# Optimization experiments

Measured on AMD Instinct MI355X. Metric: run time of the kernel, lower is better.

Reference implementation:

```python
import jax, jax.numpy as jnp
import numpy as np

P, D, K, E, ITERS, THRESH, NCLS = 16, 384, 16, 8, 10, 0.9, 1000


def _forward(x, pw, pb, ln_g, ln_b, pos, qw, qb, kw, kb, vw, vb,
             ew, eb, nw, nb, m1w, m1b, m2w, m2b, fbw, fbb, fgw, fgb, cw, cb):
    B, C, H, W = x.shape
    Hp, Wp = H // P, W // P
    # patch embedding: conv(k=s=P) == reshape + matmul; (c, ph, pw) ordering matches conv weight layout
    xp = x.reshape(B, C, Hp, P, Wp, P).transpose(0, 2, 4, 1, 3, 5).reshape(B, Hp * Wp, C * P * P)
    patches = xp @ pw + pb                                    # [B, N, D]
    # layer norm (eps=1e-5)
    mu = patches.mean(-1, keepdims=True)
    var = patches.var(-1, keepdims=True)
    pn = (patches - mu) / jnp.sqrt(var + 1e-5) * ln_g + ln_b
    # k-means (Lloyd, fixed iters, deterministic evenly-spaced init)
    N = pn.shape[1]
    init_idx = jnp.linspace(0, N - 1, K).astype(jnp.int32)
    centers0 = pn[:, init_idx]                                # [B, K, D]
    pn_sq = jnp.sum(pn * pn, -1)                              # [B, N]

    def kstep(centers, _):
        d2 = (pn_sq[:, :, None]
              - 2.0 * jnp.einsum('bnd,bkd->bnk', pn, centers)
              + jnp.sum(centers * centers, -1)[:, None, :])   # [B, N, K]
        oh = jax.nn.one_hot(jnp.argmin(d2, -1), K, dtype=pn.dtype)
        counts = oh.sum(1)                                    # [B, K]
        new = jnp.einsum('bnk,bnd->bkd', oh, pn) / jnp.maximum(counts, 1.0)[:, :, None]
        new = jnp.where(counts[:, :, None] > 0, new, centers)
        return new, None

    clusters, _ = jax.lax.scan(kstep, centers0, None, length=ITERS)  # [B, K, D]
    # attention over clusters
    clusters = clusters + pos
    Q = clusters @ qw + qb
    Kt = clusters @ kw + kb
    V = clusters @ vw + vb
    attn = jax.nn.softmax(jnp.einsum('bqd,bkd->bqk', Q, Kt) / jnp.sqrt(jnp.float32(D)), -1)
    clusters = jnp.einsum('bqk,bkd->bqd', attn, V)
    # hypergraph laplacian
    hw = jax.nn.softmax(clusters @ ew + eb, axis=1)           # [B, K, E], softmax over nodes
    Dd = hw.sum(1)                                            # [B, E]
    Hm = hw.transpose(0, 2, 1)                                # [B, E, K]
    M = (Dd ** -0.5)[:, :, None] * Hm                         # D^{-1/2} H
    L = jnp.eye(E, dtype=clusters.dtype) - jnp.einsum('bek,bfk->bef', M, Hm)  # [B, E, E]
    L = jnp.pad(L, ((0, 0), (0, K - E), (0, K - E)))          # pad to [B, K, K]
    clusters = jnp.einsum('bij,bjd->bid', L, clusters)
    clusters = clusters @ nw + nb
    # non-linear propagation MLP (exact GELU, torch default)
    clusters = jax.nn.gelu(clusters @ m1w + m1b, approximate=False) @ m2w + m2b
    # adaptive node collapse: mask from ORIGINAL clusters, sequential in-place merges
    nrm = jnp.maximum(jnp.linalg.norm(clusters, axis=-1, keepdims=True), 1e-12)
    nc = clusters / nrm
    sim = jnp.einsum('bqd,bkd->bqk', nc, nc)
    mask_any = jnp.any(sim > THRESH, axis=0)                  # [K, K]: merge pair if ANY batch exceeds
    for i in range(K):                                        # small fixed K; matches sequential torch loop
        for j in range(i + 1, K):
            cond = mask_any[i, j]
            merged = (clusters[:, i] + clusters[:, j]) * 0.5
            clusters = clusters.at[:, i].set(jnp.where(cond, merged, clusters[:, i]))
            clusters = clusters.at[:, j].set(jnp.where(cond, merged, clusters[:, j]))
    # feedback modulation
    g = clusters.mean(1)                                      # [B, D]
    fb = g @ fbw + fbb
    gate = jax.nn.sigmoid(g @ fgw + fgb)                      # [B, 1]
    clusters = clusters + fb[:, None, :] * gate[:, None, :]
    return clusters.reshape(B, -1) @ cw + cb                  # [B, num_classes]


def setup_inputs() -> dict:
    key = jax.random.key(0)
    ks = jax.random.split(key, 16)
    Wm = lambda k, *s: jax.random.normal(k, s, jnp.float32) * 0.02
    z = lambda *s: jnp.zeros(s, jnp.float32)
    return {
        'x': jax.random.normal(ks[0], (128, 3, 224, 224), jnp.float32),
        'pw': Wm(ks[1], 3 * P * P, D), 'pb': z(D),
        'ln_g': jnp.ones((D,), jnp.float32), 'ln_b': z(D),
        'pos': Wm(ks[2], K, D),
        'qw': Wm(ks[3], D, D), 'qb': z(D),
        'kw': Wm(ks[4], D, D), 'kb': z(D),
        'vw': Wm(ks[5], D, D), 'vb': z(D),
        'ew': Wm(ks[6], D, E), 'eb': z(E),
        'nw': Wm(ks[7], D, D), 'nb': z(D),
        'm1w': Wm(ks[8], D, D), 'm1b': z(D),
        'm2w': Wm(ks[9], D, D), 'm2b': z(D),
        'fbw': Wm(ks[10], D, D), 'fbb': z(D),
        'fgw': Wm(ks[11], D, 1), 'fgb': z(1),
        'cw': Wm(ks[12], D * K, NCLS), 'cb': z(NCLS),
    }


def reference(x, pw, pb, ln_g, ln_b, pos, qw, qb, kw, kb, vw, vb,
              ew, eb, nw, nb, m1w, m1b, m2w, m2b, fbw, fbb, fgw, fgb, cw, cb):
    return _forward(x, pw, pb, ln_g, ln_b, pos, qw, qb, kw, kb, vw, vb,
                    ew, eb, nw, nb, m1w, m1b, m2w, m2b, fbw, fbb, fgw, fgb, cw, cb)
```

## Files before the change

kernel.cpp:

```cpp
#include <hip/hip_runtime.h>
#include <math.h>

#define NBATCH 128
#define NPTS   196
#define DIN    768
#define DM     384
#define KCL    16
#define NEXP   8
#define NITER  10
#define NCLS   1000

__global__ __launch_bounds__(256) void init_kernel(const float* __restrict__ cb,
                                                   float* __restrict__ out,
                                                   int* __restrict__ mask) {
    int idx = blockIdx.x * 256 + threadIdx.x;
    if (idx < NBATCH * NCLS) {
        out[idx] = cb[idx % NCLS];
    } else if (idx < NBATCH * NCLS + 256) {
        mask[idx - NBATCH * NCLS] = 0;
    }
}

__global__ __launch_bounds__(256) void patch_ln_kernel(
        const float* __restrict__ x, const float* __restrict__ pw,
        const float* __restrict__ pb, const float* __restrict__ lng,
        const float* __restrict__ lnb, float* __restrict__ pn,
        float* __restrict__ pnsq) {
    __shared__ float As[32 * 32];
    __shared__ float Ws[32 * DM];
    const int tid  = threadIdx.x;
    const int m0   = blockIdx.x * 32;
    const int arow = tid >> 3, akg = tid & 7;
    const int m    = m0 + arow;
    const int bi   = m / NPTS, n = m - bi * NPTS;
    const int nh   = n / 14, nwp = n - nh * 14;
    const float* xb = x + (size_t)bi * 150528 + (size_t)(nh * 16) * 224 + nwp * 16;
    const int rg = tid >> 5, cg = tid & 31;

    float acc[4][12];
#pragma unroll
    for (int r = 0; r < 4; ++r)
#pragma unroll
        for (int j = 0; j < 12; ++j) acc[r][j] = 0.f;

    const float4* pw4 = (const float4*)pw;
    for (int kci = 0; kci < 24; ++kci) {
        {
            int k = kci * 32 + akg * 4;
            int c = k >> 8, py = (k >> 4) & 15, px = k & 15;
            float4 xv = *(const float4*)(xb + c * 50176 + py * 224 + px);
            As[(akg * 4 + 0) * 32 + arow] = xv.x;
            As[(akg * 4 + 1) * 32 + arow] = xv.y;
            As[(akg * 4 + 2) * 32 + arow] = xv.z;
            As[(akg * 4 + 3) * 32 + arow] = xv.w;
        }
#pragma unroll
        for (int t = 0; t < 12; ++t) {
            int s = tid + t * 256;
            ((float4*)Ws)[s] = pw4[kci * 3072 + s];
        }
        __syncthreads();
#pragma unroll 8
        for (int kk = 0; kk < 32; ++kk) {
            float4 a = *(const float4*)&As[kk * 32 + rg * 4];
            float w[12];
            *(float4*)&w[0] = *(const float4*)&Ws[kk * DM + cg * 12];
            *(float4*)&w[4] = *(const float4*)&Ws[kk * DM + cg * 12 + 4];
            *(float4*)&w[8] = *(const float4*)&Ws[kk * DM + cg * 12 + 8];
            float ar[4] = {a.x, a.y, a.z, a.w};
#pragma unroll
            for (int r = 0; r < 4; ++r)
#pragma unroll
                for (int j = 0; j < 12; ++j) acc[r][j] += ar[r] * w[j];
        }
        __syncthreads();
    }

    float gvv[12], bvv[12], pbv[12];
#pragma unroll
    for (int j4 = 0; j4 < 3; ++j4) {
        *(float4*)&pbv[j4 * 4] = *(const float4*)(pb + cg * 12 + j4 * 4);
        *(float4*)&gvv[j4 * 4] = *(const float4*)(lng + cg * 12 + j4 * 4);
        *(float4*)&bvv[j4 * 4] = *(const float4*)(lnb + cg * 12 + j4 * 4);
    }
#pragma unroll
    for (int r = 0; r < 4; ++r) {
        float vloc[12];
        float s = 0.f;
#pragma unroll
        for (int j = 0; j < 12; ++j) { vloc[j] = acc[r][j] + pbv[j]; s += vloc[j]; }
#pragma unroll
        for (int off = 16; off >= 1; off >>= 1) s += __shfl_xor(s, off);
        float mu = s * (1.0f / DM);
        float q = 0.f;
#pragma unroll
        for (int j = 0; j < 12; ++j) { float dd = vloc[j] - mu; q += dd * dd; }
#pragma unroll
        for (int off = 16; off >= 1; off >>= 1) q += __shfl_xor(q, off);
        float rstd = rsqrtf(q * (1.0f / DM) + 1e-5f);
        float ov[12];
        float ssq = 0.f;
#pragma unroll
        for (int j = 0; j < 12; ++j) {
            float p = (vloc[j] - mu) * rstd * gvv[j] + bvv[j];
            ov[j] = p; ssq += p * p;
        }
#pragma unroll
        for (int off = 16; off >= 1; off >>= 1) ssq += __shfl_xor(ssq, off);
        int mr = m0 + rg * 4 + r;
        float* dst = pn + (size_t)mr * DM + cg * 12;
        *(float4*)(dst)     = *(float4*)&ov[0];
        *(float4*)(dst + 4) = *(float4*)&ov[4];
        *(float4*)(dst + 8) = *(float4*)&ov[8];
        if (cg == 0) pnsq[mr] = ssq;
    }
}

__global__ __launch_bounds__(256) void kmeans_init_kernel(
        const float* __restrict__ pn, float* __restrict__ cent,
        float* __restrict__ csq, int* __restrict__ cnt) {
    const int b = blockIdx.x, tid = threadIdx.x;
    const float* pnb = pn + (size_t)b * NPTS * DM;
    float* cb = cent + (size_t)b * KCL * DM;
    for (int i = tid; i < KCL * DM / 4; i += 256) {
        int k = i / (DM / 4), d4 = i - k * (DM / 4);
        ((float4*)cb)[i] = ((const float4*)(pnb + (size_t)(13 * k) * DM))[d4];
    }
    if (tid < 128) {
        int k = tid >> 3, sub = tid & 7;
        const float* row = pnb + (size_t)(13 * k) * DM + sub * 48;
        float ss = 0.f;
        for (int d = 0; d < 48; d += 4) {
            float4 v = *(const float4*)(row + d);
            ss += v.x * v.x + v.y * v.y + v.z * v.z + v.w * v.w;
        }
#pragma unroll
        for (int off = 4; off >= 1; off >>= 1) ss += __shfl_xor(ss, off);
        if (sub == 0) csq[b * KCL + k] = ss;
    }
    if (tid < KCL) cnt[b * KCL + tid] = 0;
}

__global__ __launch_bounds__(256) void kmeans_assign_kernel(
        const float* __restrict__ pn, const float* __restrict__ pnsq,
        const float* __restrict__ cent, const float* __restrict__ csq,
        int* __restrict__ asn, int* __restrict__ cnt) {
    __shared__ float cs[KCL * DM];
    __shared__ float cq[KCL];
    const int b = blockIdx.y, tile = blockIdx.x, tid = threadIdx.x;
    const float* cb = cent + (size_t)b * KCL * DM;
    for (int i = tid; i < KCL * DM / 4; i += 256)
        ((float4*)cs)[i] = ((const float4*)cb)[i];
    if (tid < KCL) cq[tid] = csq[b * KCL + tid];
    __syncthreads();

    const int p = tid >> 3, sub = tid & 7;
    const int n = tile * 32 + p;
    if (n >= NPTS) return;
    const float4* prow = (const float4*)(pn + ((size_t)b * NPTS + n) * DM);

    float acc[KCL];
#pragma unroll
    for (int k = 0; k < KCL; ++k) acc[k] = 0.f;
#pragma unroll 2
    for (int i = 0; i < 12; ++i) {
        const int d4 = sub + 8 * i;
        float4 pv = prow[d4];
#pragma unroll
        for (int k = 0; k < KCL; ++k) {
            const float4 c = *(const float4*)&cs[k * DM + d4 * 4];
            acc[k] += pv.x * c.x + pv.y * c.y + pv.z * c.z + pv.w * c.w;
        }
    }
#pragma unroll
    for (int k = 0; k < KCL; ++k) {
        float a = acc[k];
        a += __shfl_xor(a, 1);
        a += __shfl_xor(a, 2);
        a += __shfl_xor(a, 4);
        acc[k] = a;
    }
    if (sub == 0) {
        const float mp = pnsq[b * NPTS + n];
        float best = (mp - 2.0f * acc[0]) + cq[0];
        int bk = 0;
#pragma unroll
        for (int k = 1; k < KCL; ++k) {
            float v = (mp - 2.0f * acc[k]) + cq[k];
            if (v < best) { best = v; bk = k; }
        }
        asn[b * NPTS + n] = bk;
        atomicAdd(&cnt[b * KCL + bk], 1);
    }
}

__global__ __launch_bounds__(256) void kmeans_update_kernel(
        const float* __restrict__ pn, const int* __restrict__ asn,
        int* __restrict__ cnt, float* __restrict__ cent,
        float* __restrict__ csq) {
    __shared__ unsigned long long msk[4];
    __shared__ float red[4];
    const int b = blockIdx.y, k = blockIdx.x, tid = threadIdx.x;

    int a = -1;
    if (tid < NPTS) a = asn[b * NPTS + tid];
    unsigned long long bal = __ballot(a == k);
    if ((tid & 63) == 0) msk[tid >> 6] = bal;
    __syncthreads();

    const int c = cnt[b * KCL + k];
    float sx = 0.f, sy = 0.f;
    const float* pnb = pn + (size_t)b * NPTS * DM + 2 * tid;
    if (tid < 192) {
#pragma unroll
        for (int w = 0; w < 4; ++w) {
            unsigned long long m = msk[w];
            while (m) {
                int nn = w * 64 + (int)__builtin_ctzll(m);
                m &= m - 1;
                float2 v = *(const float2*)(pnb + (size_t)nn * DM);
                sx += v.x; sy += v.y;
            }
        }
    }
    float* cr = cent + ((size_t)b * KCL + k) * DM + 2 * tid;
    float nx = 0.f, ny = 0.f;
    if (tid < 192) {
        if (c > 0) {
            float inv = 1.0f / (float)c;
            nx = sx * inv; ny = sy * inv;
        } else {
            nx = cr[0]; ny = cr[1];
        }
        cr[0] = nx; cr[1] = ny;
    }
    float ss = nx * nx + ny * ny;
#pragma unroll
    for (int off = 32; off >= 1; off >>= 1) ss += __shfl_xor(ss, off);
    if ((tid & 63) == 0) red[tid >> 6] = ss;
    __syncthreads();
    if (tid == 0) {
        csq[b * KCL + k] = red[0] + red[1] + red[2] + red[3];
        cnt[b * KCL + k] = 0;
    }
}

__global__ __launch_bounds__(256) void kmeans_finalize_kernel(
        float* __restrict__ cent, const float* __restrict__ pos) {
    int i = blockIdx.x * 256 + threadIdx.x;
    int within = i % (KCL * DM / 4);
    float4 cv = ((const float4*)cent)[i];
    float4 pv = ((const float4*)pos)[within];
    cv.x += pv.x; cv.y += pv.y; cv.z += pv.z; cv.w += pv.w;
    ((float4*)cent)[i] = cv;
}

template <int ACT>
__global__ __launch_bounds__(256) void gemm_kernel(
        const float* __restrict__ A, const float* __restrict__ W,
        const float* __restrict__ bias, float* __restrict__ out,
        int M, int N, int Kd) {
    __shared__ float As[32 * 32];
    __shared__ float Ws[32 * 128];
    const int n0 = blockIdx.x * 128;
    const int m0 = blockIdx.y * 32;
    const int tid = threadIdx.x;
    const int rg = tid >> 5, cg = tid & 31;
    const int arow = tid >> 3, akg = tid & 7;
    float acc[4][4];
#pragma unroll
    for (int r = 0; r < 4; ++r)
#pragma unroll
        for (int j = 0; j < 4; ++j) acc[r][j] = 0.f;

    for (int kc = 0; kc < Kd; kc += 32) {
        float4 av = *(const float4*)(A + (size_t)(m0 + arow) * Kd + kc + akg * 4);
        As[(akg * 4 + 0) * 32 + arow] = av.x;
        As[(akg * 4 + 1) * 32 + arow] = av.y;
        As[(akg * 4 + 2) * 32 + arow] = av.z;
        As[(akg * 4 + 3) * 32 + arow] = av.w;
#pragma unroll
        for (int t = 0; t < 4; ++t) {
            int s = tid + t * 256;
            int kk = s >> 5, c4i = s & 31;
            *(float4*)&Ws[kk * 128 + c4i * 4] =
                *(const float4*)(W + (size_t)(kc + kk) * N + n0 + c4i * 4);
        }
        __syncthreads();
#pragma unroll 16
        for (int kk = 0; kk < 32; ++kk) {
            float4 a = *(const float4*)&As[kk * 32 + rg * 4];
            float4 w = *(const float4*)&Ws[kk * 128 + cg * 4];
            float ar[4] = {a.x, a.y, a.z, a.w};
            float wr[4] = {w.x, w.y, w.z, w.w};
#pragma unroll
            for (int r = 0; r < 4; ++r)
#pragma unroll
                for (int j = 0; j < 4; ++j) acc[r][j] += ar[r] * wr[j];
        }
        __syncthreads();
    }
    float4 bv = *(const float4*)(bias + n0 + cg * 4);
    float bvr[4] = {bv.x, bv.y, bv.z, bv.w};
#pragma unroll
    for (int r = 0; r < 4; ++r) {
        float o[4];
#pragma unroll
        for (int j = 0; j < 4; ++j) {
            float v = acc[r][j] + bvr[j];
            if (ACT == 1) v = 0.5f * v * (1.0f + erff(v * 0.70710678118654752440f));
            o[j] = v;
        }
        *(float4*)(out + (size_t)(m0 + rg * 4 + r) * N + n0 + cg * 4) = *(float4*)&o[0];
    }
}

__global__ __launch_bounds__(256) void attn_spectral_kernel(
        const float* __restrict__ Qg, const float* __restrict__ Kg,
        const float* __restrict__ Vg, const float* __restrict__ ew,
        const float* __restrict__ eb, float* __restrict__ c2) {
    __shared__ float Qs[KCL * 388];
    __shared__ float Ks[KCL * 388];
    __shared__ float Ss[KCL * 17];
    __shared__ float hws[KCL * 9];
    __shared__ float rds[NEXP];
    __shared__ float Ls[NEXP * NEXP];
    const int b = blockIdx.x, tid = threadIdx.x;
    for (int idx = tid; idx < KCL * DM; idx += 256) {
        int i = idx / DM, d = idx - i * DM;
        size_t g = (size_t)b * KCL * DM + idx;
        Qs[i * 388 + d] = Qg[g];
        Ks[i * 388 + d] = Kg[g];
    }
    __syncthreads();
    {
        int i = tid >> 4, j = tid & 15;
        float acc = 0.f;
        for (int d = 0; d < DM; d += 4) {
            float4 q = *(const float4*)&Qs[i * 388 + d];
            float4 k = *(const float4*)&Ks[j * 388 + d];
            acc += q.x * k.x + q.y * k.y + q.z * k.z + q.w * k.w;
        }
        float s = acc / sqrtf((float)DM);
        float mx = s;
#pragma unroll
        for (int off = 8; off >= 1; off >>= 1) mx = fmaxf(mx, __shfl_xor(mx, off));
        float p = expf(s - mx);
        float sm = p;
#pragma unroll
        for (int off = 8; off >= 1; off >>= 1) sm += __shfl_xor(sm, off);
        Ss[i * 17 + j] = p / sm;
    }
    __syncthreads();
    for (int idx = tid; idx < KCL * DM; idx += 256) {
        int i = idx / DM, d = idx - i * DM;
        Ks[i * 388 + d] = Vg[(size_t)b * KCL * DM + idx];
    }
    __syncthreads();
    for (int idx = tid; idx < KCL * DM; idx += 256) {
        int i = idx / DM, d = idx - i * DM;
        float acc = 0.f;
#pragma unroll
        for (int j = 0; j < KCL; ++j) acc += Ss[i * 17 + j] * Ks[j * 388 + d];
        Qs[i * 388 + d] = acc;
    }
    __syncthreads();
    if (tid < 128) {
        int e = tid >> 4, i = tid & 15;
        float l = 0.f;
        for (int d = 0; d < DM; ++d) l += Qs[i * 388 + d] * ew[d * NEXP + e];
        l += eb[e];
        float mx = l;
#pragma unroll
        for (int off = 8; off >= 1; off >>= 1) mx = fmaxf(mx, __shfl_xor(mx, off));
        float p = expf(l - mx);
        float sm = p;
#pragma unroll
        for (int off = 8; off >= 1; off >>= 1) sm += __shfl_xor(sm, off);
        float h = p / sm;
        hws[i * 9 + e] = h;
        float sd = h;
#pragma unroll
        for (int off = 8; off >= 1; off >>= 1) sd += __shfl_xor(sd, off);
        if (i == 0) rds[e] = 1.0f / sqrtf(sd);
    }
    __syncthreads();
    if (tid < 64) {
        int e = tid >> 3, f = tid & 7;
        float gsum = 0.f;
#pragma unroll
        for (int k = 0; k < KCL; ++k) gsum += hws[k * 9 + e] * hws[k * 9 + f];
        Ls[e * 8 + f] = ((e == f) ? 1.0f : 0.0f) - rds[e] * gsum;
    }
    __syncthreads();
    for (int idx = tid; idx < KCL * DM; idx += 256) {
        int i = idx / DM, d = idx - i * DM;
        float acc = 0.f;
        if (i < NEXP) {
#pragma unroll
            for (int j = 0; j < NEXP; ++j) acc += Ls[i * 8 + j] * Qs[j * 388 + d];
        }
        c2[(size_t)b * KCL * DM + idx] = acc;
    }
}

__global__ __launch_bounds__(256) void simmask_kernel(const float* __restrict__ c4,
                                                      int* __restrict__ mask) {
    __shared__ float Cs[KCL * 388];
    __shared__ float rns[KCL];
    const int b = blockIdx.x, tid = threadIdx.x;
    for (int idx = tid; idx < KCL * DM; idx += 256) {
        int i = idx / DM, d = idx - i * DM;
        Cs[i * 388 + d] = c4[(size_t)b * KCL * DM + idx];
    }
    __syncthreads();
    {
        int i = tid >> 4, s = tid & 15;
        float ss = 0.f;
        for (int t = 0; t < 24; ++t) { float v = Cs[i * 388 + s + 16 * t]; ss += v * v; }
#pragma unroll
        for (int off = 8; off >= 1; off >>= 1) ss += __shfl_xor(ss, off);
        if (s == 0) rns[i] = 1.0f / fmaxf(sqrtf(ss), 1e-12f);
    }
    __syncthreads();
    for (int idx = tid; idx < KCL * DM; idx += 256) {
        int i = idx / DM, d = idx - i * DM;
        Cs[i * 388 + d] *= rns[i];
    }
    __syncthreads();
    {
        int i = tid >> 4, j = tid & 15;
        if (j > i) {
            float dp = 0.f;
            for (int d = 0; d < DM; d += 4) {
                float4 a = *(const float4*)&Cs[i * 388 + d];
                float4 c = *(const float4*)&Cs[j * 388 + d];
                dp += a.x * c.x + a.y * c.y + a.z * c.z + a.w * c.w;
            }
            if (dp > 0.9f) atomicOr(&mask[i * KCL + j], 1);
        }
    }
}

__global__ __launch_bounds__(256) void merge_fb_kernel(
        const float* __restrict__ c4, const int* __restrict__ mask,
        const float* __restrict__ fbw, const float* __restrict__ fbb,
        const float* __restrict__ fgw, const float* __restrict__ fgb,
        float* __restrict__ c5) {
    __shared__ int   mk[256];
    __shared__ float gs[DM];
    __shared__ float wred[3];
    __shared__ float gatev;
    const int b = blockIdx.x, tid = threadIdx.x;
    mk[tid] = mask[tid];
    const bool act = tid < 192;
    const int t = tid;
    float2 v[KCL];
    if (act) {
#pragma unroll
        for (int i = 0; i < KCL; ++i)
            v[i] = *(const float2*)(c4 + (size_t)b * KCL * DM + i * DM + 2 * t);
    }
    __syncthreads();
    if (act) {
#pragma unroll
        for (int i = 0; i < KCL; ++i)
#pragma unroll
            for (int j = i + 1; j < KCL; ++j)
                if (mk[i * KCL + j]) {
                    float mx = 0.5f * (v[i].x + v[j].x);
                    float my = 0.5f * (v[i].y + v[j].y);
                    v[i].x = mx; v[i].y = my; v[j].x = mx; v[j].y = my;
                }
    }
    float2 gv = {0.f, 0.f};
    if (act) {
#pragma unroll
        for (int i = 0; i < KCL; ++i) { gv.x += v[i].x; gv.y += v[i].y; }
        gv.x *= 0.0625f; gv.y *= 0.0625f;
        gs[2 * t] = gv.x; gs[2 * t + 1] = gv.y;
    }
    float pg = act ? (gv.x * fgw[2 * t] + gv.y * fgw[2 * t + 1]) : 0.f;
#pragma unroll
    for (int off = 32; off >= 1; off >>= 1) pg += __shfl_xor(pg, off);
    if (act && (tid & 63) == 0) wred[tid >> 6] = pg;
    __syncthreads();
    if (tid == 0) {
        float d = wred[0] + wred[1] + wred[2] + fgb[0];
        gatev = 1.0f / (1.0f + expf(-d));
    }
    __syncthreads();
    if (act) {
        float fx = fbb[2 * t], fy = fbb[2 * t + 1];
        for (int j = 0; j < DM; ++j) {
            float gj = gs[j];
            const float2 w = *(const float2*)(fbw + (size_t)j * DM + 2 * t);
            fx += gj * w.x; fy += gj * w.y;
        }
        float gt = gatev;
#pragma unroll
        for (int i = 0; i < KCL; ++i) {
            float2 o = {v[i].x + fx * gt, v[i].y + fy * gt};
            *(float2*)(c5 + (size_t)b * KCL * DM + i * DM + 2 * t) = o;
        }
    }
}

__global__ __launch_bounds__(256) void cls_kernel(const float* __restrict__ A,
                                                  const float* __restrict__ Wt,
                                                  float* __restrict__ out) {
    __shared__ float As[32 * 32];
    __shared__ float Ws[32 * 128];
    const int n0 = blockIdx.x * 128;
    const int m0 = blockIdx.y * 32;
    const int k0 = blockIdx.z * 768;
    const int tid = threadIdx.x;
    const int rg = tid >> 5, cg = tid & 31;
    const int arow = tid >> 3, akg = tid & 7;
    float acc[4][4];
#pragma unroll
    for (int r = 0; r < 4; ++r)
#pragma unroll
        for (int j = 0; j < 4; ++j) acc[r][j] = 0.f;

    for (int kc = k0; kc < k0 + 768; kc += 32) {
        float4 av = *(const float4*)(A + (size_t)(m0 + arow) * (KCL * DM) + kc + akg * 4);
        As[(akg * 4 + 0) * 32 + arow] = av.x;
        As[(akg * 4 + 1) * 32 + arow] = av.y;
        As[(akg * 4 + 2) * 32 + arow] = av.z;
        As[(akg * 4 + 3) * 32 + arow] = av.w;
#pragma unroll
        for (int ti = 0; ti < 4; ++ti) {
            int s = tid + ti * 256;
            int kk = s >> 5, c4i = s & 31;
            int col = n0 + c4i * 4;
            float4 wv = make_float4(0.f, 0.f, 0.f, 0.f);
            if (col < NCLS) wv = *(const float4*)(Wt + (size_t)(kc + kk) * NCLS + col);
            *(float4*)&Ws[kk * 128 + c4i * 4] = wv;
        }
        __syncthreads();
#pragma unroll 16
        for (int kk = 0; kk < 32; ++kk) {
            float4 a = *(const float4*)&As[kk * 32 + rg * 4];
            float4 w = *(const float4*)&Ws[kk * 128 + cg * 4];
            float ar[4] = {a.x, a.y, a.z, a.w};
            float wr[4] = {w.x, w.y, w.z, w.w};
#pragma unroll
            for (int r = 0; r < 4; ++r)
#pragma unroll
                for (int j = 0; j < 4; ++j) acc[r][j] += ar[r] * wr[j];
        }
        __syncthreads();
    }
    int col = n0 + cg * 4;
    if (col < NCLS) {
#pragma unroll
        for (int r = 0; r < 4; ++r) {
            int row = m0 + rg * 4 + r;
#pragma unroll
            for (int j = 0; j < 4; ++j)
                atomicAdd(&out[(size_t)row * NCLS + col + j], acc[r][j]);
        }
    }
}

extern "C" void kernel_launch(void* const* d_in, const int* in_sizes, int n_in,
                              void* d_out, int out_size, void* d_ws, size_t ws_size,
                              hipStream_t stream) {
    const float* x   = (const float*)d_in[0];
    const float* pw  = (const float*)d_in[1];
    const float* pb  = (const float*)d_in[2];
    const float* lng = (const float*)d_in[3];
    const float* lnb = (const float*)d_in[4];
    const float* pos = (const float*)d_in[5];
    const float* qw  = (const float*)d_in[6];
    const float* qb  = (const float*)d_in[7];
    const float* kw  = (const float*)d_in[8];
    const float* kb  = (const float*)d_in[9];
    const float* vw  = (const float*)d_in[10];
    const float* vb  = (const float*)d_in[11];
    const float* ew  = (const float*)d_in[12];
    const float* eb  = (const float*)d_in[13];
    const float* nw  = (const float*)d_in[14];
    const float* nb  = (const float*)d_in[15];
    const float* m1w = (const float*)d_in[16];
    const float* m1b = (const float*)d_in[17];
    const float* m2w = (const float*)d_in[18];
    const float* m2b = (const float*)d_in[19];
    const float* fbw = (const float*)d_in[20];
    const float* fbb = (const float*)d_in[21];
    const float* fgw = (const float*)d_in[22];
    const float* fgb = (const float*)d_in[23];
    const float* cw  = (const float*)d_in[24];
    const float* cb  = (const float*)d_in[25];
    float* out = (float*)d_out;
    float* ws  = (float*)d_ws;

    float* pn_   = ws;
    float* pnsq_ = ws + 9633792;
    float* c0_   = ws + 9658880;
    float* Q_    = ws + 10445312;
    float* K_    = ws + 11231744;
    float* V_    = ws + 12018176;
    float* c2_   = ws + 12804608;
    int*   mask_ = (int*)(ws + 13591040);
    float* csq_  = ws + 13591296;
    int*   cnt_  = (int*)(ws + 13593344);
    int*   asn_  = (int*)(ws + 13595392);
    float* cent_ = c0_;
    float* c3_ = Q_;
    float* h_  = K_;
    float* c4_ = V_;
    float* c5_ = c0_;

    init_kernel<<<501, 256, 0, stream>>>(cb, out, mask_);
    patch_ln_kernel<<<784, 256, 0, stream>>>(x, pw, pb, lng, lnb, pn_, pnsq_);

    kmeans_init_kernel<<<NBATCH, 256, 0, stream>>>(pn_, cent_, csq_, cnt_);
    for (int it = 0; it < NITER; ++it) {
        kmeans_assign_kernel<<<dim3(7, NBATCH), 256, 0, stream>>>(
            pn_, pnsq_, cent_, csq_, asn_, cnt_);
        kmeans_update_kernel<<<dim3(KCL, NBATCH), 256, 0, stream>>>(
            pn_, asn_, cnt_, cent_, csq_);
    }
    kmeans_finalize_kernel<<<768, 256, 0, stream>>>(cent_, pos);

    gemm_kernel<0><<<dim3(3, 64), 256, 0, stream>>>(c0_, qw, qb, Q_, 2048, DM, DM);
    gemm_kernel<0><<<dim3(3, 64), 256, 0, stream>>>(c0_, kw, kb, K_, 2048, DM, DM);
    gemm_kernel<0><<<dim3(3, 64), 256, 0, stream>>>(c0_, vw, vb, V_, 2048, DM, DM);
    attn_spectral_kernel<<<NBATCH, 256, 0, stream>>>(Q_, K_, V_, ew, eb, c2_);
    gemm_kernel<0><<<dim3(3, 64), 256, 0, stream>>>(c2_, nw, nb, c3_, 2048, DM, DM);
    gemm_kernel<1><<<dim3(3, 64), 256, 0, stream>>>(c3_, m1w, m1b, h_, 2048, DM, DM);
    gemm_kernel<0><<<dim3(3, 64), 256, 0, stream>>>(h_, m2w, m2b, c4_, 2048, DM, DM);
    simmask_kernel<<<NBATCH, 256, 0, stream>>>(c4_, mask_);
    merge_fb_kernel<<<NBATCH, 256, 0, stream>>>(c4_, mask_, fbw, fbb, fgw, fgb, c5_);
    cls_kernel<<<dim3(8, 4, 8), 256, 0, stream>>>(c5_, cw, out);
}
```

Baseline: 1.054 ms.

## Retile patch GEMM, register-block kmeans assign, fuse QKV GEMMs, stage expert weights

The patch-embedding GEMM now uses 128-thread blocks, each thread computing 8 rows by 12 columns over a K-chunk of 16. This raises register reuse per thread at the cost of fewer threads per block and higher register pressure. K-means assignment now has each thread handle 4 points over 16 dimension lanes, so each shared-memory centroid read is reused across 4 points, with fewer tiles per batch. The three Q/K/V GEMMs are fused into one launch that shares the A tile. The attention kernel transposes the expert weights into shared memory so the logit dot product uses float4 reads.

```diff
diff --git a/kernel.cpp b/kernel.cpp
--- a/kernel.cpp
+++ b/kernel.cpp
@@ -21,57 +21,59 @@
     }
 }
 
-__global__ __launch_bounds__(256) void patch_ln_kernel(
+#define BKP 16
+__global__ __launch_bounds__(128) void patch_ln_kernel(
         const float* __restrict__ x, const float* __restrict__ pw,
         const float* __restrict__ pb, const float* __restrict__ lng,
         const float* __restrict__ lnb, float* __restrict__ pn,
         float* __restrict__ pnsq) {
-    __shared__ float As[32 * 32];
-    __shared__ float Ws[32 * DM];
-    const int tid  = threadIdx.x;
-    const int m0   = blockIdx.x * 32;
-    const int arow = tid >> 3, akg = tid & 7;
-    const int m    = m0 + arow;
-    const int bi   = m / NPTS, n = m - bi * NPTS;
-    const int nh   = n / 14, nwp = n - nh * 14;
+    __shared__ float As[BKP * 36];
+    __shared__ float Ws[BKP * DM];
+    const int tid = threadIdx.x;
+    const int m0  = blockIdx.x * 32;
+    const int rg  = tid >> 5, cg = tid & 31;
+    const int lr = tid >> 2, kq = tid & 3;
+    const int m  = m0 + lr;
+    const int bi = m / NPTS, n = m - bi * NPTS;
+    const int nh = n / 14, nwp = n - nh * 14;
     const float* xb = x + (size_t)bi * 150528 + (size_t)(nh * 16) * 224 + nwp * 16;
-    const int rg = tid >> 5, cg = tid & 31;
-
-    float acc[4][12];
-#pragma unroll
-    for (int r = 0; r < 4; ++r)
+
+    float acc[8][12];
+#pragma unroll
+    for (int r = 0; r < 8; ++r)
 #pragma unroll
         for (int j = 0; j < 12; ++j) acc[r][j] = 0.f;
 
     const float4* pw4 = (const float4*)pw;
-    for (int kci = 0; kci < 24; ++kci) {
+    for (int kc = 0; kc < DIN; kc += BKP) {
         {
-            int k = kci * 32 + akg * 4;
+            int k = kc + kq * 4;
             int c = k >> 8, py = (k >> 4) & 15, px = k & 15;
             float4 xv = *(const float4*)(xb + c * 50176 + py * 224 + px);
-            As[(akg * 4 + 0) * 32 + arow] = xv.x;
-            As[(akg * 4 + 1) * 32 + arow] = xv.y;
-            As[(akg * 4 + 2) * 32 + arow] = xv.z;
-            As[(akg * 4 + 3) * 32 + arow] = xv.w;
+            As[(kq * 4 + 0) * 36 + lr] = xv.x;
+            As[(kq * 4 + 1) * 36 + lr] = xv.y;
+            As[(kq * 4 + 2) * 36 + lr] = xv.z;
+            As[(kq * 4 + 3) * 36 + lr] = xv.w;
         }
 #pragma unroll
         for (int t = 0; t < 12; ++t) {
-            int s = tid + t * 256;
-            ((float4*)Ws)[s] = pw4[kci * 3072 + s];
+            int s = tid + t * 128;
+            ((float4*)Ws)[s] = pw4[kc * 96 + s];
         }
         __syncthreads();
-#pragma unroll 8
-        for (int kk = 0; kk < 32; ++kk) {
-            float4 a = *(const float4*)&As[kk * 32 + rg * 4];
+#pragma unroll 4
+        for (int kk = 0; kk < BKP; ++kk) {
+            float a[8];
+            *(float4*)&a[0] = *(const float4*)&As[kk * 36 + rg * 8];
+            *(float4*)&a[4] = *(const float4*)&As[kk * 36 + rg * 8 + 4];
             float w[12];
             *(float4*)&w[0] = *(const float4*)&Ws[kk * DM + cg * 12];
             *(float4*)&w[4] = *(const float4*)&Ws[kk * DM + cg * 12 + 4];
             *(float4*)&w[8] = *(const float4*)&Ws[kk * DM + cg * 12 + 8];
-            float ar[4] = {a.x, a.y, a.z, a.w};
-#pragma unroll
-            for (int r = 0; r < 4; ++r)
-#pragma unroll
-                for (int j = 0; j < 12; ++j) acc[r][j] += ar[r] * w[j];
+#pragma unroll
+            for (int r = 0; r < 8; ++r)
+#pragma unroll
+                for (int j = 0; j < 12; ++j) acc[r][j] += a[r] * w[j];
         }
         __syncthreads();
     }
@@ -84,7 +86,7 @@
         *(float4*)&bvv[j4 * 4] = *(const float4*)(lnb + cg * 12 + j4 * 4);
     }
 #pragma unroll
-    for (int r = 0; r < 4; ++r) {
+    for (int r = 0; r < 8; ++r) {
         float vloc[12];
         float s = 0.f;
 #pragma unroll
@@ -107,7 +109,7 @@
         }
 #pragma unroll
         for (int off = 16; off >= 1; off >>= 1) ssq += __shfl_xor(ssq, off);
-        int mr = m0 + rg * 4 + r;
+        int mr = m0 + rg * 8 + r;
         float* dst = pn + (size_t)mr * DM + cg * 12;
         *(float4*)(dst)     = *(float4*)&ov[0];
         *(float4*)(dst + 4) = *(float4*)&ov[4];
@@ -149,48 +151,65 @@
     __shared__ float cq[KCL];
     const int b = blockIdx.y, tile = blockIdx.x, tid = threadIdx.x;
     const float* cb = cent + (size_t)b * KCL * DM;
-    for (int i = tid; i < KCL * DM / 4; i += 256)
-        ((float4*)cs)[i] = ((const float4*)cb)[i];
+    for (int t = 0; t < 6; ++t)
+        ((float4*)cs)[tid + t * 256] = ((const float4*)cb)[tid + t * 256];
     if (tid < KCL) cq[tid] = csq[b * KCL + tid];
     __syncthreads();
 
-    const int p = tid >> 3, sub = tid & 7;
-    const int n = tile * 32 + p;
-    if (n >= NPTS) return;
-    const float4* prow = (const float4*)(pn + ((size_t)b * NPTS + n) * DM);
-
-    float acc[KCL];
-#pragma unroll
-    for (int k = 0; k < KCL; ++k) acc[k] = 0.f;
-#pragma unroll 2
-    for (int i = 0; i < 12; ++i) {
-        const int d4 = sub + 8 * i;
-        float4 pv = prow[d4];
+    const int sub = tid & 15, pg = tid >> 4;
+    const int n0 = tile * 64 + pg * 4;
+    const float* prow[4];
+#pragma unroll
+    for (int pp = 0; pp < 4; ++pp) {
+        int np = n0 + pp; if (np > NPTS - 1) np = NPTS - 1;
+        prow[pp] = pn + ((size_t)b * NPTS + np) * DM;
+    }
+
+    float acc[KCL][4];
+#pragma unroll
+    for (int k = 0; k < KCL; ++k)
+#pragma unroll
+        for (int pp = 0; pp < 4; ++pp) acc[k][pp] = 0.f;
+
+    for (int i = 0; i < 6; ++i) {
+        const int d4 = sub + 16 * i;
+        float4 pv[4];
+#pragma unroll
+        for (int pp = 0; pp < 4; ++pp) pv[pp] = ((const float4*)prow[pp])[d4];
 #pragma unroll
         for (int k = 0; k < KCL; ++k) {
             const float4 c = *(const float4*)&cs[k * DM + d4 * 4];
-            acc[k] += pv.x * c.x + pv.y * c.y + pv.z * c.z + pv.w * c.w;
-        }
-    }
-#pragma unroll
-    for (int k = 0; k < KCL; ++k) {
-        float a = acc[k];
-        a += __shfl_xor(a, 1);
-        a += __shfl_xor(a, 2);
-        a += __shfl_xor(a, 4);
-        acc[k] = a;
-    }
-    if (sub == 0) {
-        const float mp = pnsq[b * NPTS + n];
-        float best = (mp - 2.0f * acc[0]) + cq[0];
-        int bk = 0;
-#pragma unroll
-        for (int k = 1; k < KCL; ++k) {
-            float v = (mp - 2.0f * acc[k]) + cq[k];
-            if (v < best) { best = v; bk = k; }
-        }
-        asn[b * NPTS + n] = bk;
-        atomicAdd(&cnt[b * KCL + bk], 1);
+#pragma unroll
+            for (int pp = 0; pp < 4; ++pp)
+                acc[k][pp] += pv[pp].x * c.x + pv[pp].y * c.y +
+                              pv[pp].z * c.z + pv[pp].w * c.w;
+        }
+    }
+#pragma unroll
+    for (int k = 0; k < KCL; ++k)
+#pragma unroll
+        for (int pp = 0; pp < 4; ++pp) {
+            float a = acc[k][pp];
+            a += __shfl_xor(a, 1);
+            a += __shfl_xor(a, 2);
+            a += __shfl_xor(a, 4);
+            a += __shfl_xor(a, 8);
+            acc[k][pp] = a;
+        }
+    if (sub < 4) {
+        const int pp = sub, n = n0 + pp;
+        if (n < NPTS) {
+            const float mp = pnsq[b * NPTS + n];
+            float best = (mp - 2.0f * acc[0][pp]) + cq[0];
+            int bk = 0;
+#pragma unroll
+            for (int k = 1; k < KCL; ++k) {
+                float v = (mp - 2.0f * acc[k][pp]) + cq[k];
+                if (v < best) { best = v; bk = k; }
+            }
+            asn[b * NPTS + n] = bk;
+            atomicAdd(&cnt[b * KCL + bk], 1);
+        }
     }
 }
 
@@ -253,6 +272,79 @@
     float4 pv = ((const float4*)pos)[within];
     cv.x += pv.x; cv.y += pv.y; cv.z += pv.z; cv.w += pv.w;
     ((float4*)cent)[i] = cv;
+}
+
+__global__ __launch_bounds__(256) void gemm_qkv_kernel(
+        const float* __restrict__ A,
+        const float* __restrict__ qw, const float* __restrict__ kw,
+        const float* __restrict__ vw,
+        const float* __restrict__ qb, const float* __restrict__ kb,
+        const float* __restrict__ vb,
+        float* __restrict__ Q, float* __restrict__ K, float* __restrict__ V) {
+    __shared__ float As[32 * 32];
+    __shared__ float Ws[3][32 * 128];
+    const int n0 = blockIdx.x * 128;
+    const int m0 = blockIdx.y * 32;
+    const int tid = threadIdx.x;
+    const int rg = tid >> 5, cg = tid & 31;
+    const int arow = tid >> 3, akg = tid & 7;
+    const float* W[3] = {qw, kw, vw};
+
+    float acc[3][4][4];
+#pragma unroll
+    for (int g = 0; g < 3; ++g)
+#pragma unroll
+        for (int r = 0; r < 4; ++r)
+#pragma unroll
+            for (int j = 0; j < 4; ++j) acc[g][r][j] = 0.f;
+
+    for (int kc = 0; kc < DM; kc += 32) {
+        float4 av = *(const float4*)(A + (size_t)(m0 + arow) * DM + kc + akg * 4);
+        As[(akg * 4 + 0) * 32 + arow] = av.x;
+        As[(akg * 4 + 1) * 32 + arow] = av.y;
+        As[(akg * 4 + 2) * 32 + arow] = av.z;
+        As[(akg * 4 + 3) * 32 + arow] = av.w;
+#pragma unroll
+        for (int g = 0; g < 3; ++g)
+#pragma unroll
+            for (int t = 0; t < 4; ++t) {
+                int s = tid + t * 256;
+                int kk = s >> 5, c4i = s & 31;
+                *(float4*)&Ws[g][kk * 128 + c4i * 4] =
+                    *(const float4*)(W[g] + (size_t)(kc + kk) * DM + n0 + c4i * 4);
+            }
+        __syncthreads();
+#pragma unroll 8
+        for (int kk = 0; kk < 32; ++kk) {
+            float4 a = *(const float4*)&As[kk * 32 + rg * 4];
+            float ar[4] = {a.x, a.y, a.z, a.w};
+#pragma unroll
+            for (int g = 0; g < 3; ++g) {
+                float4 w = *(const float4*)&Ws[g][kk * 128 + cg * 4];
+                float wr[4] = {w.x, w.y, w.z, w.w};
+#pragma unroll
+                for (int r = 0; r < 4; ++r)
+#pragma unroll
+                    for (int j = 0; j < 4; ++j) acc[g][r][j] += ar[r] * wr[j];
+            }
+        }
+        __syncthreads();
+    }
+    const float* B[3] = {qb, kb, vb};
+    float* O[3] = {Q, K, V};
+#pragma unroll
+    for (int g = 0; g < 3; ++g) {
+        float4 bv = *(const float4*)(B[g] + n0 + cg * 4);
+        float bvr[4] = {bv.x, bv.y, bv.z, bv.w};
+#pragma unroll
+        for (int r = 0; r < 4; ++r) {
+            float o[4];
+#pragma unroll
+            for (int j = 0; j < 4; ++j) o[j] = acc[g][r][j] + bvr[j];
+            *(float4*)(O[g] + (size_t)(m0 + rg * 4 + r) * DM + n0 + cg * 4) =
+                *(float4*)&o[0];
+        }
+    }
 }
 
 template <int ACT>
@@ -321,6 +413,7 @@
         const float* __restrict__ eb, float* __restrict__ c2) {
     __shared__ float Qs[KCL * 388];
     __shared__ float Ks[KCL * 388];
+    __shared__ float ewt[NEXP * 388];
     __shared__ float Ss[KCL * 17];
     __shared__ float hws[KCL * 9];
     __shared__ float rds[NEXP];
@@ -332,6 +425,10 @@
         Qs[i * 388 + d] = Qg[g];
         Ks[i * 388 + d] = Kg[g];
     }
+    for (int idx = tid; idx < DM * NEXP; idx += 256) {
+        int d = idx >> 3, e = idx & 7;
+        ewt[e * 388 + d] = ew[idx];
+    }
     __syncthreads();
     {
         int i = tid >> 4, j = tid & 15;
@@ -368,7 +465,11 @@
     if (tid < 128) {
         int e = tid >> 4, i = tid & 15;
         float l = 0.f;
-        for (int d = 0; d < DM; ++d) l += Qs[i * 388 + d] * ew[d * NEXP + e];
+        for (int d4 = 0; d4 < DM / 4; ++d4) {
+            float4 q = *(const float4*)&Qs[i * 388 + d4 * 4];
+            float4 w = *(const float4*)&ewt[e * 388 + d4 * 4];
+            l += q.x * w.x + q.y * w.y + q.z * w.z + q.w * w.w;
+        }
         l += eb[e];
         float mx = l;
 #pragma unroll
@@ -614,20 +715,19 @@
     float* c5_ = c0_;
 
     init_kernel<<<501, 256, 0, stream>>>(cb, out, mask_);
-    patch_ln_kernel<<<784, 256, 0, stream>>>(x, pw, pb, lng, lnb, pn_, pnsq_);
+    patch_ln_kernel<<<784, 128, 0, stream>>>(x, pw, pb, lng, lnb, pn_, pnsq_);
 
     kmeans_init_kernel<<<NBATCH, 256, 0, stream>>>(pn_, cent_, csq_, cnt_);
     for (int it = 0; it < NITER; ++it) {
-        kmeans_assign_kernel<<<dim3(7, NBATCH), 256, 0, stream>>>(
+        kmeans_assign_kernel<<<dim3(4, NBATCH), 256, 0, stream>>>(
             pn_, pnsq_, cent_, csq_, asn_, cnt_);
         kmeans_update_kernel<<<dim3(KCL, NBATCH), 256, 0, stream>>>(
             pn_, asn_, cnt_, cent_, csq_);
     }
     kmeans_finalize_kernel<<<768, 256, 0, stream>>>(cent_, pos);
 
-    gemm_kernel<0><<<dim3(3, 64), 256, 0, stream>>>(c0_, qw, qb, Q_, 2048, DM, DM);
-    gemm_kernel<0><<<dim3(3, 64), 256, 0, stream>>>(c0_, kw, kb, K_, 2048, DM, DM);
-    gemm_kernel<0><<<dim3(3, 64), 256, 0, stream>>>(c0_, vw, vb, V_, 2048, DM, DM);
+    gemm_qkv_kernel<<<dim3(3, 64), 256, 0, stream>>>(c0_, qw, kw, vw, qb, kb, vb,
+                                                     Q_, K_, V_);
     attn_spectral_kernel<<<NBATCH, 256, 0, stream>>>(Q_, K_, V_, ew, eb, c2_);
     gemm_kernel<0><<<dim3(3, 64), 256, 0, stream>>>(c2_, nw, nb, c3_, 2048, DM, DM);
     gemm_kernel<1><<<dim3(3, 64), 256, 0, stream>>>(c3_, m1w, m1b, h_, 2048, DM, DM);
```

Measured after the change: 1.244 ms. 18.1% more time.
